# Optimization experiments

Measured on AMD Instinct MI355X. Metric: run time of the kernel, lower is better.

The kernel has to match this reference:

```python
import jax, jax.numpy as jnp
import numpy as np

HIDDEN_DIM = 2048
NUM_CONN = int(HIDDEN_DIM * HIDDEN_DIM * 0.1)  # 419430


def setup_inputs() -> dict:
    key = jax.random.key(0)
    k1, k2, k3 = jax.random.split(key, 3)
    x = jax.random.normal(k1, (4, 2048, HIDDEN_DIM), dtype=jnp.float32)
    connection_indices = jax.random.randint(k2, (2, NUM_CONN), 0, HIDDEN_DIM, dtype=jnp.int64)
    connection_values = jax.random.normal(k3, (NUM_CONN,), dtype=jnp.float32) * 0.001
    alpha = jnp.asarray(0.01, dtype=jnp.float32)
    return {"x": x, "connection_indices": connection_indices,
            "connection_values": connection_values, "alpha": alpha}


def reference(x, connection_indices, connection_values, alpha):
    # Rebuild dense W from COO (duplicate indices sum, matching sparse_coo_tensor.to_dense())
    H = x.shape[-1]
    W = jnp.zeros((H, H), dtype=x.dtype).at[connection_indices[0], connection_indices[1]].add(connection_values)
    # torch.matmul(x, W.T): out[b,s,i] = sum_j x[b,s,j] * W[i,j]
    lateral = jnp.einsum('bsj,ij->bsi', x, W)
    return x + alpha * lateral
```

## Files before the change

kernel.cpp:

```cpp
#include <hip/hip_runtime.h>


typedef unsigned short u16;
typedef __attribute__((ext_vector_type(8))) short bf16x8;
typedef __attribute__((ext_vector_type(4))) float f32x4;

#define HID 2048
#define BM 128
#define BN 128
#define BK 32

__device__ __forceinline__ u16 f2bf(float f) {
    unsigned u = __builtin_bit_cast(unsigned, f);
    u += 0x7fffu + ((u >> 16) & 1u);
    return (u16)(u >> 16);
}

__global__ void cvt_f32_bf16_kernel(const float* __restrict__ in,
                                    u16* __restrict__ out, int n8) {
    int stride = gridDim.x * blockDim.x;
    for (int i = blockIdx.x * blockDim.x + threadIdx.x; i < n8; i += stride) {
        const float4* p = (const float4*)in + (size_t)i * 2;
        float4 a = p[0], b = p[1];
        uint4 o;
        o.x = (unsigned)f2bf(a.x) | ((unsigned)f2bf(a.y) << 16);
        o.y = (unsigned)f2bf(a.z) | ((unsigned)f2bf(a.w) << 16);
        o.z = (unsigned)f2bf(b.x) | ((unsigned)f2bf(b.y) << 16);
        o.w = (unsigned)f2bf(b.z) | ((unsigned)f2bf(b.w) << 16);
        ((uint4*)out)[i] = o;
    }
}

__global__ void scatter_coo_kernel(const int* __restrict__ idx,
                                   const float* __restrict__ vals,
                                   float* __restrict__ W, int nnz) {
    int n = blockIdx.x * blockDim.x + threadIdx.x;
    if (n < nnz) {
        int i = idx[n];
        int j = idx[nnz + n];
        atomicAdd(W + (size_t)i * HID + j, vals[n]);
    }
}

#define GLDS(gsrc, ldst)                                                   \
    __builtin_amdgcn_global_load_lds(                                      \
        (const __attribute__((address_space(1))) void*)(gsrc),             \
        (__attribute__((address_space(3))) void*)(ldst), 16, 0, 0)

__global__ __launch_bounds__(256) void gemm_bt_kernel(
        const u16* __restrict__ A, const u16* __restrict__ B,
        const float* __restrict__ Xf, const float* __restrict__ alphap,
        float* __restrict__ out, int M) {
    __shared__ u16 As[BM * BK];
    __shared__ u16 Bs[BN * BK];

    const int t = threadIdx.x;
    const int lane = t & 63;
    const int w = t >> 6;
    const int wr = w >> 1, wc = w & 1;
    const int fr = lane & 15;
    const int kg = lane >> 4;

    const int nwg = gridDim.x;
    const int cpx = nwg >> 3;
    const int bid = blockIdx.x;
    const int swz = (bid & 7) * cpx + (bid >> 3);
    const int nbn = HID / BN;
    const int bm = swz / nbn;
    const int bn = swz % nbn;
    const size_t rowBase = (size_t)bm * BM;
    const size_t colBase = (size_t)bn * BN;

    const int lrow = lane >> 2;
    const int lcol = (lane & 3) * 8;

    f32x4 acc[4][4] = {};

    const int KT = HID / BK;
    for (int kt = 0; kt < KT; ++kt) {
        const int k0 = kt * BK;
#pragma unroll
        for (int p = 0; p < 2; ++p) {
            const int chunk = (p << 2) + w;
            const int row = (chunk << 4) + lrow;
            GLDS(A + (rowBase + row) * HID + k0 + lcol, &As[chunk * 512 + lane * 8]);
            GLDS(B + (colBase + row) * HID + k0 + lcol, &Bs[chunk * 512 + lane * 8]);
        }
        __syncthreads();

        bf16x8 af[4], bfv[4];
#pragma unroll
        for (int mi = 0; mi < 4; ++mi)
            af[mi] = *(const bf16x8*)&As[(wr * 64 + mi * 16 + fr) * BK + kg * 8];
#pragma unroll
        for (int ni = 0; ni < 4; ++ni)
            bfv[ni] = *(const bf16x8*)&Bs[(wc * 64 + ni * 16 + fr) * BK + kg * 8];
#pragma unroll
        for (int mi = 0; mi < 4; ++mi)
#pragma unroll
            for (int ni = 0; ni < 4; ++ni)
                acc[mi][ni] = __builtin_amdgcn_mfma_f32_16x16x32_bf16(
                    af[mi], bfv[ni], acc[mi][ni], 0, 0, 0);
        __syncthreads();
    }

    const float alphav = *alphap;
#pragma unroll
    for (int mi = 0; mi < 4; ++mi) {
#pragma unroll
        for (int ni = 0; ni < 4; ++ni) {
            f32x4 c = acc[mi][ni];
            const size_t gn = colBase + wc * 64 + ni * 16 + fr;
#pragma unroll
            for (int r = 0; r < 4; ++r) {
                const size_t gm = rowBase + wr * 64 + mi * 16 + kg * 4 + r;
                const size_t o = gm * HID + gn;
                out[o] = Xf[o] + alphav * c[r];
            }
        }
    }
}

extern "C" void kernel_launch(void* const* d_in, const int* in_sizes, int n_in,
                              void* d_out, int out_size, void* d_ws, size_t ws_size,
                              hipStream_t stream) {
    const float* x     = (const float*)d_in[0];
    const int*   idx   = (const int*)d_in[1];
    const float* vals  = (const float*)d_in[2];
    const float* alpha = (const float*)d_in[3];
    float* out = (float*)d_out;

    const int nnz = in_sizes[2];
    const int M = in_sizes[0] / HID;

    float* Wf = (float*)d_ws;
    u16*   Xb = (u16*)d_ws;
    u16*   Wb = (u16*)((char*)d_ws + (size_t)32 * 1024 * 1024);

    hipMemsetAsync(Wf, 0, (size_t)HID * HID * sizeof(float), stream);
    scatter_coo_kernel<<<(nnz + 255) / 256, 256, 0, stream>>>(idx, vals, Wf, nnz);

    cvt_f32_bf16_kernel<<<2048, 256, 0, stream>>>(Wf, Wb, (HID * HID) / 8);

    cvt_f32_bf16_kernel<<<2048, 256, 0, stream>>>(x, Xb, (M * HID) / 8);

    const int grid = (M / BM) * (HID / BN);
    gemm_bt_kernel<<<grid, 256, 0, stream>>>(Xb, Wb, x, alpha, out, M);
}
```

Baseline: 242.5 us.

## Use 256x256 tiles with 4-stage LDS pipeline, swizzled LDS, and fused conversion

```diff
diff --git a/kernel.cpp b/kernel.cpp
--- a/kernel.cpp
+++ b/kernel.cpp
@@ -6,9 +6,12 @@
 typedef __attribute__((ext_vector_type(4))) float f32x4;
 
 #define HID 2048
-#define BM 128
-#define BN 128
+#define BM 256
+#define BN 256
 #define BK 32
+#define NT (HID / BK)
+#define SLOT_ELEMS (BM * BK + BN * BK)
+#define HALF_ELEMS (128 * BK)
 
 __device__ __forceinline__ u16 f2bf(float f) {
     unsigned u = __builtin_bit_cast(unsigned, f);
@@ -16,18 +19,34 @@
     return (u16)(u >> 16);
 }
 
+__device__ __forceinline__ void cvt8(const float* __restrict__ src,
+                                     u16* __restrict__ dst, int i) {
+    const float4* p = (const float4*)src + (size_t)i * 2;
+    float4 a = p[0], b = p[1];
+    uint4 o;
+    o.x = (unsigned)f2bf(a.x) | ((unsigned)f2bf(a.y) << 16);
+    o.y = (unsigned)f2bf(a.z) | ((unsigned)f2bf(a.w) << 16);
+    o.z = (unsigned)f2bf(b.x) | ((unsigned)f2bf(b.y) << 16);
+    o.w = (unsigned)f2bf(b.z) | ((unsigned)f2bf(b.w) << 16);
+    ((uint4*)dst)[i] = o;
+}
+
 __global__ void cvt_f32_bf16_kernel(const float* __restrict__ in,
                                     u16* __restrict__ out, int n8) {
     int stride = gridDim.x * blockDim.x;
-    for (int i = blockIdx.x * blockDim.x + threadIdx.x; i < n8; i += stride) {
-        const float4* p = (const float4*)in + (size_t)i * 2;
-        float4 a = p[0], b = p[1];
-        uint4 o;
-        o.x = (unsigned)f2bf(a.x) | ((unsigned)f2bf(a.y) << 16);
-        o.y = (unsigned)f2bf(a.z) | ((unsigned)f2bf(a.w) << 16);
-        o.z = (unsigned)f2bf(b.x) | ((unsigned)f2bf(b.y) << 16);
-        o.w = (unsigned)f2bf(b.z) | ((unsigned)f2bf(b.w) << 16);
-        ((uint4*)out)[i] = o;
+    for (int i = blockIdx.x * blockDim.x + threadIdx.x; i < n8; i += stride)
+        cvt8(in, out, i);
+}
+
+__global__ void cvt_both_kernel(const float* __restrict__ w,
+                                const float* __restrict__ x,
+                                u16* __restrict__ wb, u16* __restrict__ xb,
+                                int n8w, int n8x) {
+    int stride = gridDim.x * blockDim.x;
+    int total = n8w + n8x;
+    for (int i = blockIdx.x * blockDim.x + threadIdx.x; i < total; i += stride) {
+        if (i < n8w) cvt8(w, wb, i);
+        else         cvt8(x, xb, i - n8w);
     }
 }
 
@@ -47,75 +66,123 @@
         (const __attribute__((address_space(1))) void*)(gsrc),             \
         (__attribute__((address_space(3))) void*)(ldst), 16, 0, 0)
 
-__global__ __launch_bounds__(256) void gemm_bt_kernel(
-        const u16* __restrict__ A, const u16* __restrict__ B,
-        const float* __restrict__ Xf, const float* __restrict__ alphap,
-        float* __restrict__ out, int M) {
-    __shared__ u16 As[BM * BK];
-    __shared__ u16 Bs[BN * BK];
+__global__ __launch_bounds__(512, 2) void gemm8_kernel(
+        const u16* __restrict__ A,
+        const u16* __restrict__ B,
+        const float* __restrict__ Xf,
+        const float* __restrict__ alphap,
+        float* __restrict__ out) {
+    __shared__ u16 lds[4 * SLOT_ELEMS];
 
     const int t = threadIdx.x;
     const int lane = t & 63;
     const int w = t >> 6;
-    const int wr = w >> 1, wc = w & 1;
+    const int wr = w >> 2;
+    const int wc = w & 3;
     const int fr = lane & 15;
     const int kg = lane >> 4;
 
-    const int nwg = gridDim.x;
-    const int cpx = nwg >> 3;
     const int bid = blockIdx.x;
-    const int swz = (bid & 7) * cpx + (bid >> 3);
-    const int nbn = HID / BN;
-    const int bm = swz / nbn;
-    const int bn = swz % nbn;
+    const int swz = (bid & 7) * 32 + (bid >> 3);
+    const int bm = swz >> 3;
+    const int bn = swz & 7;
     const size_t rowBase = (size_t)bm * BM;
     const size_t colBase = (size_t)bn * BN;
 
-    const int lrow = lane >> 2;
-    const int lcol = (lane & 3) * 8;
-
-    f32x4 acc[4][4] = {};
-
-    const int KT = HID / BK;
-    for (int kt = 0; kt < KT; ++kt) {
-        const int k0 = kt * BK;
-#pragma unroll
-        for (int p = 0; p < 2; ++p) {
-            const int chunk = (p << 2) + w;
-            const int row = (chunk << 4) + lrow;
-            GLDS(A + (rowBase + row) * HID + k0 + lcol, &As[chunk * 512 + lane * 8]);
-            GLDS(B + (colBase + row) * HID + k0 + lcol, &Bs[chunk * 512 + lane * 8]);
+    const int srow = (w << 4) + (lane >> 2);
+    const int sg = (lane & 3) ^ ((srow >> 1) & 3);
+    const u16* aSrc = A + (rowBase + srow) * HID + sg * 8;
+    const u16* bSrc = B + (colBase + srow) * HID + sg * 8;
+    const int ldst = (w << 9) + (lane << 3);
+
+    const int gread = kg ^ ((fr >> 1) & 3);
+
+    f32x4 acc[8][4] = {};
+
+    for (int pt = 0; pt < 3; ++pt) {
+        u16* slot = lds + (pt & 3) * SLOT_ELEMS;
+        const u16* as = aSrc + pt * BK;
+        const u16* bs = bSrc + pt * BK;
+        GLDS(as,             slot + ldst);
+        GLDS(bs,             slot + 2 * HALF_ELEMS + ldst);
+        GLDS(as + 128 * HID, slot + HALF_ELEMS + ldst);
+        GLDS(bs + 128 * HID, slot + 3 * HALF_ELEMS + ldst);
+    }
+    asm volatile("s_waitcnt vmcnt(8)" ::: "memory");
+    __builtin_amdgcn_s_barrier();
+    __builtin_amdgcn_sched_barrier(0);
+
+#pragma unroll 1
+    for (int tt = 0; tt < NT; ++tt) {
+        u16* slot  = lds + (tt & 3) * SLOT_ELEMS;
+        u16* slot3 = lds + ((tt + 3) & 3) * SLOT_ELEMS;
+        const int t3 = tt + 3;
+        const u16* as3 = aSrc + t3 * BK;
+        const u16* bs3 = bSrc + t3 * BK;
+        const u16* aRd = slot + (wr * 128 + fr) * BK + gread * 8;
+        const u16* bRd = slot + 2 * HALF_ELEMS + (wc * 64 + fr) * BK + gread * 8;
+
+        bf16x8 b[4];
+
+        bf16x8 a0[4];
+#pragma unroll
+        for (int m = 0; m < 4; ++m)
+            a0[m] = *(const bf16x8*)(aRd + m * 16 * BK);
+#pragma unroll
+        for (int n = 0; n < 4; ++n)
+            b[n] = *(const bf16x8*)(bRd + n * 16 * BK);
+        if (t3 < NT) {
+            GLDS(as3, slot3 + ldst);
+            GLDS(bs3, slot3 + 2 * HALF_ELEMS + ldst);
         }
-        __syncthreads();
-
-        bf16x8 af[4], bfv[4];
-#pragma unroll
-        for (int mi = 0; mi < 4; ++mi)
-            af[mi] = *(const bf16x8*)&As[(wr * 64 + mi * 16 + fr) * BK + kg * 8];
-#pragma unroll
-        for (int ni = 0; ni < 4; ++ni)
-            bfv[ni] = *(const bf16x8*)&Bs[(wc * 64 + ni * 16 + fr) * BK + kg * 8];
-#pragma unroll
-        for (int mi = 0; mi < 4; ++mi)
-#pragma unroll
-            for (int ni = 0; ni < 4; ++ni)
-                acc[mi][ni] = __builtin_amdgcn_mfma_f32_16x16x32_bf16(
-                    af[mi], bfv[ni], acc[mi][ni], 0, 0, 0);
-        __syncthreads();
+        asm volatile("s_waitcnt lgkmcnt(0)" ::: "memory");
+        __builtin_amdgcn_s_barrier();
+        __builtin_amdgcn_sched_barrier(0);
+        __builtin_amdgcn_s_setprio(1);
+#pragma unroll
+        for (int m = 0; m < 4; ++m)
+#pragma unroll
+            for (int n = 0; n < 4; ++n)
+                acc[m][n] = __builtin_amdgcn_mfma_f32_16x16x32_bf16(
+                    a0[m], b[n], acc[m][n], 0, 0, 0);
+        __builtin_amdgcn_s_setprio(0);
+
+        bf16x8 a1[4];
+#pragma unroll
+        for (int m = 0; m < 4; ++m)
+            a1[m] = *(const bf16x8*)(aRd + (m + 4) * 16 * BK);
+        if (t3 < NT) {
+            GLDS(as3 + 128 * HID, slot3 + HALF_ELEMS + ldst);
+            GLDS(bs3 + 128 * HID, slot3 + 3 * HALF_ELEMS + ldst);
+        }
+        asm volatile("s_waitcnt lgkmcnt(0)" ::: "memory");
+        if (tt < NT - 3)       asm volatile("s_waitcnt vmcnt(8)" ::: "memory");
+        else if (tt == NT - 3) asm volatile("s_waitcnt vmcnt(4)" ::: "memory");
+        else if (tt == NT - 2) asm volatile("s_waitcnt vmcnt(0)" ::: "memory");
+        __builtin_amdgcn_s_barrier();
+        __builtin_amdgcn_sched_barrier(0);
+        __builtin_amdgcn_s_setprio(1);
+#pragma unroll
+        for (int m = 0; m < 4; ++m)
+#pragma unroll
+            for (int n = 0; n < 4; ++n)
+                acc[m + 4][n] = __builtin_amdgcn_mfma_f32_16x16x32_bf16(
+                    a1[m], b[n], acc[m + 4][n], 0, 0, 0);
+        __builtin_amdgcn_s_setprio(0);
     }
 
     const float alphav = *alphap;
 #pragma unroll
-    for (int mi = 0; mi < 4; ++mi) {
-#pragma unroll
-        for (int ni = 0; ni < 4; ++ni) {
-            f32x4 c = acc[mi][ni];
-            const size_t gn = colBase + wc * 64 + ni * 16 + fr;
-#pragma unroll
-            for (int r = 0; r < 4; ++r) {
-                const size_t gm = rowBase + wr * 64 + mi * 16 + kg * 4 + r;
+    for (int m = 0; m < 8; ++m) {
+#pragma unroll
+        for (int n = 0; n < 4; ++n) {
+            f32x4 c = acc[m][n];
+            const size_t gn = colBase + wc * 64 + n * 16 + fr;
+#pragma unroll
+            for (int j = 0; j < 4; ++j) {
+                const size_t gm = rowBase + wr * 128 + m * 16 + kg * 4 + j;
                 const size_t o = gm * HID + gn;
-                out[o] = Xf[o] + alphav * c[r];
+                out[o] = Xf[o] + alphav * c[j];
             }
         }
     }
@@ -131,19 +198,26 @@
     float* out = (float*)d_out;
 
     const int nnz = in_sizes[2];
-    const int M = in_sizes[0] / HID;
-
-    float* Wf = (float*)d_ws;
-    u16*   Xb = (u16*)d_ws;
-    u16*   Wb = (u16*)((char*)d_ws + (size_t)32 * 1024 * 1024);
-
-    hipMemsetAsync(Wf, 0, (size_t)HID * HID * sizeof(float), stream);
-    scatter_coo_kernel<<<(nnz + 255) / 256, 256, 0, stream>>>(idx, vals, Wf, nnz);
-
-    cvt_f32_bf16_kernel<<<2048, 256, 0, stream>>>(Wf, Wb, (HID * HID) / 8);
-
-    cvt_f32_bf16_kernel<<<2048, 256, 0, stream>>>(x, Xb, (M * HID) / 8);
-
-    const int grid = (M / BM) * (HID / BN);
-    gemm_bt_kernel<<<grid, 256, 0, stream>>>(Xb, Wb, x, alpha, out, M);
-}
+    const size_t MB = 1024 * 1024;
+    const int n8W = (HID * HID) / 8;
+    const int n8X = in_sizes[0] / 8;
+
+    if (ws_size >= 56 * MB) {
+        u16*   Xb = (u16*)d_ws;
+        u16*   Wb = (u16*)((char*)d_ws + 32 * MB);
+        float* Wf = (float*)((char*)d_ws + 40 * MB);
+        hipMemsetAsync(Wf, 0, (size_t)HID * HID * sizeof(float), stream);
+        scatter_coo_kernel<<<(nnz + 255) / 256, 256, 0, stream>>>(idx, vals, Wf, nnz);
+        cvt_both_kernel<<<2048, 256, 0, stream>>>(Wf, x, Wb, Xb, n8W, n8X);
+        gemm8_kernel<<<256, 512, 0, stream>>>(Xb, Wb, x, alpha, out);
+    } else {
+        float* Wf = (float*)d_ws;
+        u16*   Xb = (u16*)d_ws;
+        u16*   Wb = (u16*)((char*)d_ws + 32 * MB);
+        hipMemsetAsync(Wf, 0, (size_t)HID * HID * sizeof(float), stream);
+        scatter_coo_kernel<<<(nnz + 255) / 256, 256, 0, stream>>>(idx, vals, Wf, nnz);
+        cvt_f32_bf16_kernel<<<2048, 256, 0, stream>>>(Wf, Wb, n8W);
+        cvt_f32_bf16_kernel<<<2048, 256, 0, stream>>>(x, Xb, n8X);
+        gemm8_kernel<<<256, 512, 0, stream>>>(Xb, Wb, x, alpha, out);
+    }
+}
```

Measured after the change: 212.0 us. -12.6%, faster.
